# Kernel tuning notes

Measured on AMD Instinct MI355X. Metric: run time of the kernel, lower is better.

Reference implementation:

```python
import jax, jax.numpy as jnp
import numpy as np
from jax import lax

UNIT = 0.11  # pairing threshold from sort_w(weight, 0.11)


def _greedy_pairs(wflat, unit=UNIT):
    """Faithful greedy pairing from sort_w: for each out-channel dd, scan flat
    indices a ascending; pair a with the first unoccupied b>a with
    |w[a]+w[b]|<=unit. Returns gather indices src and signs such that
    Weff[dd,i] = sign[dd,i] * Wflat[dd, src[dd,i]] reproduces vicsum_v2."""
    d, m = wflat.shape
    src = np.tile(np.arange(m, dtype=np.int32), (d, 1))
    sign = np.ones((d, m), dtype=np.float32)
    for dd in range(d):
        occ = np.zeros(m, dtype=bool)
        row = wflat[dd]
        for a in range(m - 1):
            if occ[a]:
                continue
            cand = np.nonzero((~occ[a + 1:]) & (np.abs(row[a] + row[a + 1:]) <= unit))[0]
            if cand.size:
                b = a + 1 + int(cand[0])
                occ[a] = occ[b] = True
                src[dd, b] = a     # out += (x[a]-x[b])*w[a]  =>  coeff at b is -w[a]
                sign[dd, b] = -1.0
    return src, sign


def _make_conv(rng, d, c, k):
    bound = 1.0 / np.sqrt(c * k * k)  # torch default uniform init scale
    w = rng.uniform(-bound, bound, size=(d, c, k, k)).astype(np.float32)
    b = rng.uniform(-bound, bound, size=(d,)).astype(np.float32)
    src, sign = _greedy_pairs(w.reshape(d, -1))
    return w, b, src, sign


def setup_inputs() -> dict:
    rng = np.random.default_rng(0)
    x = rng.standard_normal((16384, 1, 32, 32)).astype(np.float32)
    w1, b1, src1, sign1 = _make_conv(rng, 6, 1, 5)
    w2, b2, src2, sign2 = _make_conv(rng, 16, 6, 5)
    w3, b3, src3, sign3 = _make_conv(rng, 120, 16, 5)
    bf1 = 1.0 / np.sqrt(120.0)
    fc1_w = rng.uniform(-bf1, bf1, size=(84, 120)).astype(np.float32)
    fc1_b = rng.uniform(-bf1, bf1, size=(84,)).astype(np.float32)
    bf2 = 1.0 / np.sqrt(84.0)
    fc2_w = rng.uniform(-bf2, bf2, size=(10, 84)).astype(np.float32)
    fc2_b = rng.uniform(-bf2, bf2, size=(10,)).astype(np.float32)
    return {
        'x': jnp.asarray(x),
        'w1': jnp.asarray(w1), 'b1': jnp.asarray(b1), 'sign1': jnp.asarray(sign1),
        'w2': jnp.asarray(w2), 'b2': jnp.asarray(b2), 'sign2': jnp.asarray(sign2),
        'w3': jnp.asarray(w3), 'b3': jnp.asarray(b3), 'sign3': jnp.asarray(sign3),
        'fc1_w': jnp.asarray(fc1_w), 'fc1_b': jnp.asarray(fc1_b),
        'fc2_w': jnp.asarray(fc2_w), 'fc2_b': jnp.asarray(fc2_b),
        'src1': jnp.asarray(src1), 'src2': jnp.asarray(src2), 'src3': jnp.asarray(src3),
        'TRIGGERed': 1, 'count': 0,
    }


def _eff_weight(w, src, sign):
    d = w.shape[0]
    wflat = w.reshape(d, -1)
    weff = jnp.take_along_axis(wflat, src, axis=1) * sign
    return weff.reshape(w.shape)


def _conv(x, w, b):
    y = lax.conv_general_dilated(x, w, window_strides=(1, 1), padding='VALID',
                                 dimension_numbers=('NCHW', 'OIHW', 'NCHW'))
    return y + b[None, :, None, None]


def _avgpool2(x):
    n, c, h, w = x.shape
    return x.reshape(n, c, h // 2, 2, w // 2, 2).mean(axis=(3, 5))


def reference(x, w1, b1, sign1, w2, b2, sign2, w3, b3, sign3,
              fc1_w, fc1_b, fc2_w, fc2_b, src1, src2, src3, TRIGGERed, count):
    if TRIGGERed:
        h = _avgpool2(jax.nn.sigmoid(_conv(x, _eff_weight(w1, src1, sign1), b1)))
        h = _avgpool2(jax.nn.sigmoid(_conv(h, _eff_weight(w2, src2, sign2), b2)))
        h = jax.nn.sigmoid(_conv(h, _eff_weight(w3, src3, sign3), b3))
    else:
        h = _avgpool2(jax.nn.sigmoid(_conv(x, w1, b1)))
        h = _avgpool2(jax.nn.sigmoid(_conv(h, w2, b2)))
        h = jax.nn.sigmoid(_conv(h, w3, b3))
    h = h.reshape(h.shape[0], -1)                     # [N, 120]
    h = jax.nn.sigmoid(h @ fc1_w.T + fc1_b)           # [N, 84]
    return h @ fc2_w.T + fc2_b                        # [N, 10]
```

## Files before the change

### kernel.cpp

```cpp
#include <hip/hip_runtime.h>

#define THREADS 256

typedef _Float16 half2v __attribute__((ext_vector_type(2)));
typedef __fp16   half2p __attribute__((ext_vector_type(2)));

__device__ __forceinline__ float sigmoidf(float x) {
    return __builtin_amdgcn_rcpf(1.0f + __expf(-x));
}

__device__ __forceinline__ half2v f2h2(float f) {
    union { float f; half2v h; } u; u.f = f; return u.h;
}

__device__ __forceinline__ half2v pk2h2(half2p p) {
    union { half2p p; half2v h; } u; u.p = p; return u.h;
}

#define E2OFF 168
#define E3OFF 2856
#define P1OFF 54056

__global__ void weff_prep(const float* __restrict__ w1, const float* __restrict__ sg1, const int* __restrict__ sr1,
                          const float* __restrict__ w2, const float* __restrict__ sg2, const int* __restrict__ sr2,
                          const float* __restrict__ w3, const float* __restrict__ sg3, const int* __restrict__ sr3,
                          const int* __restrict__ trig, float* __restrict__ ws) {
    int i = blockIdx.x * blockDim.x + threadIdx.x;
    const int t = trig[0];
    if (i < 168) {
        int c = i / 28, k = i % 28;
        float v = 0.f;
        if (k < 25) { int f = c * 25 + k; v = t ? sg1[f] * w1[c * 25 + sr1[f]] : w1[f]; }
        ws[i] = v;
    } else if (i < 1704) {
        int j = i - E2OFF;
        int oc = j / 96, r = j % 96, ic = r / 16, slot = r % 16;
        const int base = oc * 150 + ic * 25;
        float outv = 0.f;
        if (slot < 10) {
            int kx = slot >> 1, p = slot & 1;
            int k0 = base + (2 * p) * 5 + kx;
            int k1 = base + (2 * p + 1) * 5 + kx;
            float v0 = t ? sg2[k0] * w2[oc * 150 + sr2[k0]] : w2[k0];
            float v1 = t ? sg2[k1] * w2[oc * 150 + sr2[k1]] : w2[k1];
            union { _Float16 h[2]; float f; } pun;
            pun.h[0] = (_Float16)v0;
            pun.h[1] = (_Float16)v1;
            outv = pun.f;
        } else if (slot < 15) {
            int kx = slot - 10;
            int k4 = base + 20 + kx;
            outv = t ? sg2[k4] * w2[oc * 150 + sr2[k4]] : w2[k4];
        }
        ws[i] = outv;
    } else if (i < E3OFF) {
        ws[i] = 0.f;
    } else if (i < P1OFF) {
        int idx = i - E3OFF;
        if (idx < 48000) {
            int q  = idx & 3;
            int j  = (idx >> 2) & 1;
            int tt = (idx >> 3) % 120;
            int k  = idx / 960;
            int c  = 2 * (tt >> 1) + j;
            int h  = tt & 1;
            int e  = c * 400 + h * 200 + 4 * k + q;
            ws[i] = t ? sg3[e] * w3[c * 400 + sr3[e]] : w3[e];
        } else {
            ws[i] = 0.f;
        }
    }
}

__global__ __launch_bounds__(THREADS, 4)
void k_conv1(const float* __restrict__ x, const float* __restrict__ ws,
             const float* __restrict__ b1, float* __restrict__ p1, int nimg) {
    __shared__ __align__(16) float lw[176];
    const int tid = threadIdx.x;
    if (tid < 168) lw[tid] = ws[tid];
    if (tid >= 168 && tid < 174) lw[tid] = b1[tid - 168];
    __syncthreads();

    int g = blockIdx.x * THREADS + tid;
    if (g >= nimg * 98) return;
    const int img = g / 98, rem = g % 98;
    const int r = rem / 7, t = rem % 7;

    const float* xb = x + (size_t)img * 1024 + (2 * r) * 32 + 4 * t;
    float pt[6][8];
    #pragma unroll
    for (int rr = 0; rr < 6; ++rr) {
        const float4 v0 = *reinterpret_cast<const float4*>(xb + rr * 32);
        const float4 v1 = *reinterpret_cast<const float4*>(xb + rr * 32 + 4);
        pt[rr][0] = v0.x; pt[rr][1] = v0.y; pt[rr][2] = v0.z; pt[rr][3] = v0.w;
        pt[rr][4] = v1.x; pt[rr][5] = v1.y; pt[rr][6] = v1.z; pt[rr][7] = v1.w;
    }

    #pragma unroll
    for (int c = 0; c < 6; ++c) {
        float z[2][4];
        #pragma unroll
        for (int p = 0; p < 2; ++p)
            #pragma unroll
            for (int w = 0; w < 4; ++w) z[p][w] = 0.f;

        #pragma unroll
        for (int k4 = 0; k4 < 6; ++k4) {
            const float4 w4 = *reinterpret_cast<const float4*>(&lw[c * 28 + 4 * k4]);
            #pragma unroll
            for (int j = 0; j < 4; ++j) {
                const int k = 4 * k4 + j;
                const int ky = k / 5, kx = k % 5;
                const float wv = (j == 0) ? w4.x : (j == 1) ? w4.y : (j == 2) ? w4.z : w4.w;
                #pragma unroll
                for (int p = 0; p < 2; ++p)
                    #pragma unroll
                    for (int dy = 0; dy < 2; ++dy)
                        #pragma unroll
                        for (int dx = 0; dx < 2; ++dx)
                            z[p][2 * dy + dx] += pt[dy + ky][2 * p + dx + kx] * wv;
            }
        }
        {
            const float wv = lw[c * 28 + 24];
            #pragma unroll
            for (int p = 0; p < 2; ++p)
                #pragma unroll
                for (int dy = 0; dy < 2; ++dy)
                    #pragma unroll
                    for (int dx = 0; dx < 2; ++dx)
                        z[p][2 * dy + dx] += pt[dy + 4][2 * p + dx + 4] * wv;
        }

        const float bb = lw[168 + c];
        const float s0 = sigmoidf(z[0][0] + bb) + sigmoidf(z[0][1] + bb) +
                         sigmoidf(z[0][2] + bb) + sigmoidf(z[0][3] + bb);
        const float s1 = sigmoidf(z[1][0] + bb) + sigmoidf(z[1][1] + bb) +
                         sigmoidf(z[1][2] + bb) + sigmoidf(z[1][3] + bb);
        *reinterpret_cast<float2*>(&p1[((size_t)img * 6 + c) * 196 + r * 14 + 2 * t]) =
            make_float2(0.25f * s0, 0.25f * s1);
    }
}

__global__ __launch_bounds__(THREADS, 3)
void k_conv2(const float* __restrict__ p1, const float* __restrict__ ws,
             const float* __restrict__ b2, float* __restrict__ p2, int nimg) {
    int g = blockIdx.x * THREADS + threadIdx.x;
    if (g >= nimg * 50) return;
    const int img = g / 50, rem = g % 50;
    const int pix = rem >> 1, di = rem & 1;
    const int pi = pix / 5, pj = pix % 5;
    const float* pimg = p1 + (size_t)img * 1176 + (2 * pi + di) * 14 + 2 * pj;
    const float* wq = ws + E2OFF;

    float acc[16][2];
    #pragma unroll
    for (int oc = 0; oc < 16; ++oc) { acc[oc][0] = 0.f; acc[oc][1] = 0.f; }

    for (int ic = 0; ic < 6; ++ic) {
        float pt[5][6];
        const float* pb = pimg + ic * 196;
        #pragma unroll
        for (int r = 0; r < 5; ++r) {
            #pragma unroll
            for (int cc = 0; cc < 3; ++cc) {
                float2 v = *reinterpret_cast<const float2*>(pb + r * 14 + 2 * cc);
                pt[r][2 * cc] = v.x; pt[r][2 * cc + 1] = v.y;
            }
        }
        half2v pk01[6], pk23[6];
        #pragma unroll
        for (int cc = 0; cc < 6; ++cc) {
            pk01[cc] = pk2h2(__builtin_amdgcn_cvt_pkrtz(pt[0][cc], pt[1][cc]));
            pk23[cc] = pk2h2(__builtin_amdgcn_cvt_pkrtz(pt[2][cc], pt[3][cc]));
        }
        #pragma unroll
        for (int oc = 0; oc < 16; ++oc) {
            const float* wrow = wq + (oc * 6 + ic) * 16;
            #pragma unroll
            for (int kx = 0; kx < 5; ++kx) {
                const half2v wa = f2h2(wrow[2 * kx]);
                const half2v wb = f2h2(wrow[2 * kx + 1]);
                const float  wf = wrow[10 + kx];
                acc[oc][0] = __builtin_amdgcn_fdot2(pk01[kx], wa, acc[oc][0], false);
                acc[oc][0] = __builtin_amdgcn_fdot2(pk23[kx], wb, acc[oc][0], false);
                acc[oc][0] += pt[4][kx] * wf;
                acc[oc][1] = __builtin_amdgcn_fdot2(pk01[kx + 1], wa, acc[oc][1], false);
                acc[oc][1] = __builtin_amdgcn_fdot2(pk23[kx + 1], wb, acc[oc][1], false);
                acc[oc][1] += pt[4][kx + 1] * wf;
            }
        }
    }

    #pragma unroll
    for (int oc = 0; oc < 16; ++oc) {
        const float bb = b2[oc];
        float s = sigmoidf(acc[oc][0] + bb) + sigmoidf(acc[oc][1] + bb);
        s += __shfl_xor(s, 1, 64);
        if (di == 0)
            p2[(size_t)img * 400 + oc * 25 + pix] = 0.25f * s;
    }
}

#define T_IMG 8
__global__ __launch_bounds__(128, 4)
void k_tail(const float* __restrict__ p2, const float* __restrict__ ws,
            const float* __restrict__ b3,
            const float* __restrict__ fc1w, const float* __restrict__ fc1b,
            const float* __restrict__ fc2w, const float* __restrict__ fc2b,
            float* __restrict__ out, int nimg) {
    __shared__ __align__(16) float sp2[T_IMG][400];
    __shared__ __align__(16) float v3[T_IMG][120];
    __shared__ __align__(16) float v4[T_IMG][84];
    const int tid = threadIdx.x;
    const int img0 = blockIdx.x * T_IMG;

    for (int i = tid; i < T_IMG * 100; i += 128) {
        const int im = i / 100, off = i % 100;
        const int gi = min(img0 + im, nimg - 1);
        reinterpret_cast<float4*>(&sp2[im][0])[off] =
            reinterpret_cast<const float4*>(p2 + (size_t)gi * 400)[off];
    }
    __syncthreads();

    if (tid < 120) {
        const int h = tid & 1;
        const int cpair = tid >> 1;
        float acc[2][T_IMG];
        #pragma unroll
        for (int j = 0; j < 2; ++j)
            #pragma unroll
            for (int im = 0; im < T_IMG; ++im) acc[j][im] = 0.f;

        const float4* wp = reinterpret_cast<const float4*>(ws + E3OFF);
        #pragma unroll 2
        for (int k = 0; k < 50; ++k) {
            const float4 w0 = wp[(k * 120 + tid) * 2];
            const float4 w1 = wp[(k * 120 + tid) * 2 + 1];
            #pragma unroll
            for (int im = 0; im < T_IMG; ++im) {
                const float4 u = *reinterpret_cast<const float4*>(&sp2[im][h * 200 + 4 * k]);
                acc[0][im] += w0.x * u.x + w0.y * u.y + w0.z * u.z + w0.w * u.w;
                acc[1][im] += w1.x * u.x + w1.y * u.y + w1.z * u.z + w1.w * u.w;
            }
        }
        #pragma unroll
        for (int j = 0; j < 2; ++j) {
            const int c = 2 * cpair + j;
            const float bb = b3[c];
            #pragma unroll
            for (int im = 0; im < T_IMG; ++im) {
                float s = acc[j][im];
                s += __shfl_xor(s, 1, 64);
                if (h == 0) v3[im][c] = sigmoidf(s + bb);
            }
        }
    }
    __syncthreads();

    for (int it = tid; it < T_IMG * 84; it += 128) {
        const int im = it / 84, j = it % 84;
        const float4* wp = reinterpret_cast<const float4*>(fc1w + j * 120);
        const float4* vp = reinterpret_cast<const float4*>(&v3[im][0]);
        float4 a = make_float4(0.f, 0.f, 0.f, 0.f);
        #pragma unroll 6
        for (int k = 0; k < 30; ++k) {
            const float4 w4 = wp[k];
            const float4 u = vp[k];
            a.x += u.x * w4.x; a.y += u.y * w4.y;
            a.z += u.z * w4.z; a.w += u.w * w4.w;
        }
        v4[im][j] = sigmoidf((a.x + a.y) + (a.z + a.w) + fc1b[j]);
    }
    __syncthreads();

    if (tid < T_IMG * 10) {
        const int im = tid / 10, j = tid % 10;
        if (img0 + im < nimg) {
            const float4* wp = reinterpret_cast<const float4*>(fc2w + j * 84);
            const float4* vp = reinterpret_cast<const float4*>(&v4[im][0]);
            float4 a = make_float4(0.f, 0.f, 0.f, 0.f);
            #pragma unroll
            for (int k = 0; k < 21; ++k) {
                const float4 w4 = wp[k];
                const float4 u = vp[k];
                a.x += u.x * w4.x; a.y += u.y * w4.y;
                a.z += u.z * w4.z; a.w += u.w * w4.w;
            }
            out[(size_t)(img0 + im) * 10 + j] = (a.x + a.y) + (a.z + a.w) + fc2b[j];
        }
    }
}

__device__ __forceinline__ float wget_ig(const float* __restrict__ wp,
                                         const float* __restrict__ sg,
                                         const int* __restrict__ sr,
                                         int row, int m, int idx, bool tg) {
    int f = row * m + idx;
    return tg ? sg[f] * wp[row * m + sr[f]] : wp[f];
}

__global__ __launch_bounds__(THREADS, 4)
void lenet_fused(const float* __restrict__ x,
                 const float* __restrict__ w1e, const float* __restrict__ b1,
                 const float* __restrict__ w2e, const float* __restrict__ b2,
                 const float* __restrict__ w3e, const float* __restrict__ b3,
                 const float* __restrict__ fc1w, const float* __restrict__ fc1b,
                 const float* __restrict__ fc2w, const float* __restrict__ fc2b,
                 const float* __restrict__ sg1, const int* __restrict__ sr1,
                 const float* __restrict__ sg2, const int* __restrict__ sr2,
                 const float* __restrict__ sg3, const int* __restrict__ sr3,
                 const int* __restrict__ trig,
                 float* __restrict__ out, int nimg) {
    const int tid = threadIdx.x;
    const int img0 = blockIdx.x * 2;
    __shared__ __align__(16) float xs[2][1024];
    __shared__ __align__(16) float p1[2][6][196];
    __shared__ __align__(16) float p2[2][400];
    __shared__ __align__(16) float v3[2][120];
    __shared__ __align__(16) float v4[2][84];
    const bool tg = trig[0] != 0;

    #pragma unroll
    for (int im = 0; im < 2; ++im) {
        int gi = min(img0 + im, nimg - 1);
        reinterpret_cast<float4*>(&xs[im][0])[tid] =
            reinterpret_cast<const float4*>(x + (size_t)gi * 1024)[tid];
    }
    __syncthreads();

    for (int it = tid; it < 2 * 196; it += THREADS) {
        const int img = it / 196, pix = it % 196;
        const int pi = pix / 14, pj = pix % 14;
        const float* xb = &xs[img][(2 * pi) * 32 + 2 * pj];
        float pt[6][6];
        #pragma unroll
        for (int r = 0; r < 6; ++r)
            #pragma unroll
            for (int cc = 0; cc < 3; ++cc) {
                float2 v = *reinterpret_cast<const float2*>(&xb[r * 32 + cc * 2]);
                pt[r][cc * 2] = v.x; pt[r][cc * 2 + 1] = v.y;
            }
        #pragma unroll
        for (int c = 0; c < 6; ++c) {
            float z0 = 0.f, z1 = 0.f, z2 = 0.f, z3 = 0.f;
            #pragma unroll
            for (int ky = 0; ky < 5; ++ky)
                #pragma unroll
                for (int kx = 0; kx < 5; ++kx) {
                    const float wv = wget_ig(w1e, sg1, sr1, c, 25, ky * 5 + kx, tg);
                    z0 += pt[ky][kx] * wv;     z1 += pt[ky][kx + 1] * wv;
                    z2 += pt[ky + 1][kx] * wv; z3 += pt[ky + 1][kx + 1] * wv;
                }
            const float bb = b1[c];
            p1[img][c][pix] = 0.25f * (sigmoidf(z0 + bb) + sigmoidf(z1 + bb) +
                                       sigmoidf(z2 + bb) + sigmoidf(z3 + bb));
        }
    }
    __syncthreads();

    if (tid < 200) {
        const int img = tid / 100, rem = tid % 100;
        const int pix = rem >> 2, win = rem & 3;
        const int di = win >> 1, dj = win & 1;
        const int pi = pix / 5, pj = pix % 5;
        const int r0 = 2 * pi + di, c0 = 2 * pj + dj;
        float acc[16];
        #pragma unroll
        for (int c = 0; c < 16; ++c) acc[c] = 0.f;
        for (int ic = 0; ic < 6; ++ic) {
            float pt[5][5];
            #pragma unroll
            for (int ky = 0; ky < 5; ++ky)
                #pragma unroll
                for (int kx = 0; kx < 5; ++kx)
                    pt[ky][kx] = p1[img][ic][(r0 + ky) * 14 + (c0 + kx)];
            #pragma unroll
            for (int c = 0; c < 16; ++c) {
                float z = acc[c];
                #pragma unroll
                for (int ky = 0; ky < 5; ++ky)
                    #pragma unroll
                    for (int kx = 0; kx < 5; ++kx)
                        z += pt[ky][kx] * wget_ig(w2e, sg2, sr2, c, 150, ic * 25 + ky * 5 + kx, tg);
                acc[c] = z;
            }
        }
        #pragma unroll
        for (int c = 0; c < 16; ++c) {
            float z = sigmoidf(acc[c] + b2[c]);
            z += __shfl_xor(z, 1, 64);
            z += __shfl_xor(z, 2, 64);
            if (win == 0) p2[img][c * 25 + pix] = 0.25f * z;
        }
    }
    __syncthreads();

    if (tid < 240) {
        const int c = tid >> 1, h = tid & 1;
        float s0 = 0.f, s1 = 0.f;
        for (int k = 0; k < 200; ++k) {
            float wv = wget_ig(w3e, sg3, sr3, c, 400, h * 200 + k, tg);
            s0 += p2[0][h * 200 + k] * wv;
            s1 += p2[1][h * 200 + k] * wv;
        }
        s0 += __shfl_xor(s0, 1, 64);
        s1 += __shfl_xor(s1, 1, 64);
        if (h == 0) {
            const float bb = b3[c];
            v3[0][c] = sigmoidf(s0 + bb);
            v3[1][c] = sigmoidf(s1 + bb);
        }
    }
    __syncthreads();

    if (tid < 168) {
        const int img = tid / 84, j = tid % 84;
        float a = 0.f;
        for (int k = 0; k < 120; ++k) a += v3[img][k] * fc1w[j * 120 + k];
        v4[img][j] = sigmoidf(a + fc1b[j]);
    }
    __syncthreads();

    if (tid < 20) {
        const int img = tid / 10, j = tid % 10;
        if (img0 + img < nimg) {
            float a = 0.f;
            for (int k = 0; k < 84; ++k) a += v4[img][k] * fc2w[j * 84 + k];
            out[(size_t)(img0 + img) * 10 + j] = a + fc2b[j];
        }
    }
}

extern "C" void kernel_launch(void* const* d_in, const int* in_sizes, int n_in,
                              void* d_out, int out_size, void* d_ws, size_t ws_size,
                              hipStream_t stream) {
    const float* x    = (const float*)d_in[0];
    const float* w1   = (const float*)d_in[1];
    const float* b1   = (const float*)d_in[2];
    const float* sg1  = (const float*)d_in[3];
    const float* w2   = (const float*)d_in[4];
    const float* b2   = (const float*)d_in[5];
    const float* sg2  = (const float*)d_in[6];
    const float* w3   = (const float*)d_in[7];
    const float* b3   = (const float*)d_in[8];
    const float* sg3  = (const float*)d_in[9];
    const float* fc1w = (const float*)d_in[10];
    const float* fc1b = (const float*)d_in[11];
    const float* fc2w = (const float*)d_in[12];
    const float* fc2b = (const float*)d_in[13];
    const int*   sr1  = (const int*)d_in[14];
    const int*   sr2  = (const int*)d_in[15];
    const int*   sr3  = (const int*)d_in[16];
    const int*   trig = (const int*)d_in[17];

    const int nimg = in_sizes[0] / 1024;
    float* out = (float*)d_out;

    const size_t p1off = P1OFF;
    const size_t p2off = p1off + (size_t)nimg * 1176;
    const size_t need_bytes = (p2off + (size_t)nimg * 400) * sizeof(float);

    if (ws_size >= need_bytes) {
        float* ws = (float*)d_ws;
        weff_prep<<<(P1OFF + 255) / 256, 256, 0, stream>>>(
            w1, sg1, sr1, w2, sg2, sr2, w3, sg3, sr3, trig, ws);
        k_conv1<<<(nimg * 98 + THREADS - 1) / THREADS, THREADS, 0, stream>>>(
            x, ws, b1, ws + p1off, nimg);
        k_conv2<<<(nimg * 50 + THREADS - 1) / THREADS, THREADS, 0, stream>>>(
            ws + p1off, ws, b2, ws + p2off, nimg);
        k_tail<<<(nimg + T_IMG - 1) / T_IMG, 128, 0, stream>>>(
            ws + p2off, ws, b3, fc1w, fc1b, fc2w, fc2b, out, nimg);
    } else {
        lenet_fused<<<(nimg + 1) / 2, THREADS, 0, stream>>>(
            x, w1, b1, w2, b2, w3, b3,
            fc1w, fc1b, fc2w, fc2b, sg1, sr1, sg2, sr2, sg3, sr3, trig, out, nimg);
    }
}
```

Baseline: 220.0 us.

## Store conv2 pooled output as packed fp16 and use fdot2 in conv3

```diff
diff --git a/kernel.cpp b/kernel.cpp
--- a/kernel.cpp
+++ b/kernel.cpp
@@ -15,6 +15,10 @@
 
 __device__ __forceinline__ half2v pk2h2(half2p p) {
     union { half2p p; half2v h; } u; u.p = p; return u.h;
+}
+
+__device__ __forceinline__ float h2pf(half2p p) {
+    union { half2p p; float f; } u; u.p = p; return u.f;
 }
 
 #define E2OFF 168
@@ -55,20 +59,30 @@
         ws[i] = outv;
     } else if (i < E3OFF) {
         ws[i] = 0.f;
+    } else if (i < 26856) {
+        int idx = i - E3OFF;
+        int q   = idx & 3;
+        int ch  = (idx >> 2) & 1;
+        int tt  = (idx >> 3) % 120;
+        int j4  = idx / 960;
+        int h   = tt & 1;
+        int cpair = tt >> 1;
+        int c   = 2 * cpair + ch;
+        int s   = h * 100 + 4 * j4 + q;
+        int ocp = s / 25, pix = s % 25;
+        int e0  = (2 * ocp) * 25 + pix;
+        int e1  = (2 * ocp + 1) * 25 + pix;
+        float v0 = t ? sg3[c * 400 + e0 - (c * 400 + e0) + c * 400 + e0] * 0.f : 0.f;
+        int f0 = c * 400 + e0;
+        int f1 = c * 400 + e1;
+        v0 = t ? sg3[f0] * w3[c * 400 + sr3[f0]] : w3[f0];
+        float v1 = t ? sg3[f1] * w3[c * 400 + sr3[f1]] : w3[f1];
+        union { _Float16 hh[2]; float f; } pun;
+        pun.hh[0] = (_Float16)v0;
+        pun.hh[1] = (_Float16)v1;
+        ws[i] = pun.f;
     } else if (i < P1OFF) {
-        int idx = i - E3OFF;
-        if (idx < 48000) {
-            int q  = idx & 3;
-            int j  = (idx >> 2) & 1;
-            int tt = (idx >> 3) % 120;
-            int k  = idx / 960;
-            int c  = 2 * (tt >> 1) + j;
-            int h  = tt & 1;
-            int e  = c * 400 + h * 200 + 4 * k + q;
-            ws[i] = t ? sg3[e] * w3[c * 400 + sr3[e]] : w3[e];
-        } else {
-            ws[i] = 0.f;
-        }
+        ws[i] = 0.f;
     }
 }
 
@@ -144,7 +158,7 @@
 
 __global__ __launch_bounds__(THREADS, 3)
 void k_conv2(const float* __restrict__ p1, const float* __restrict__ ws,
-             const float* __restrict__ b2, float* __restrict__ p2, int nimg) {
+             const float* __restrict__ b2, float* __restrict__ p2h, int nimg) {
     int g = blockIdx.x * THREADS + threadIdx.x;
     if (g >= nimg * 50) return;
     const int img = g / 50, rem = g % 50;
@@ -192,34 +206,41 @@
         }
     }
 
+    float pooled[16];
     #pragma unroll
     for (int oc = 0; oc < 16; ++oc) {
         const float bb = b2[oc];
         float s = sigmoidf(acc[oc][0] + bb) + sigmoidf(acc[oc][1] + bb);
         s += __shfl_xor(s, 1, 64);
-        if (di == 0)
-            p2[(size_t)img * 400 + oc * 25 + pix] = 0.25f * s;
+        pooled[oc] = 0.25f * s;
+    }
+    if (di == 0) {
+        #pragma unroll
+        for (int ocp = 0; ocp < 8; ++ocp) {
+            p2h[(size_t)img * 200 + ocp * 25 + pix] =
+                h2pf(__builtin_amdgcn_cvt_pkrtz(pooled[2 * ocp], pooled[2 * ocp + 1]));
+        }
     }
 }
 
 #define T_IMG 8
 __global__ __launch_bounds__(128, 4)
-void k_tail(const float* __restrict__ p2, const float* __restrict__ ws,
+void k_tail(const float* __restrict__ p2h, const float* __restrict__ ws,
             const float* __restrict__ b3,
             const float* __restrict__ fc1w, const float* __restrict__ fc1b,
             const float* __restrict__ fc2w, const float* __restrict__ fc2b,
             float* __restrict__ out, int nimg) {
-    __shared__ __align__(16) float sp2[T_IMG][400];
+    __shared__ __align__(16) float sp2[T_IMG][200];
     __shared__ __align__(16) float v3[T_IMG][120];
     __shared__ __align__(16) float v4[T_IMG][84];
     const int tid = threadIdx.x;
     const int img0 = blockIdx.x * T_IMG;
 
-    for (int i = tid; i < T_IMG * 100; i += 128) {
-        const int im = i / 100, off = i % 100;
+    for (int i = tid; i < T_IMG * 50; i += 128) {
+        const int im = i / 50, off = i % 50;
         const int gi = min(img0 + im, nimg - 1);
         reinterpret_cast<float4*>(&sp2[im][0])[off] =
-            reinterpret_cast<const float4*>(p2 + (size_t)gi * 400)[off];
+            reinterpret_cast<const float4*>(p2h + (size_t)gi * 200)[off];
     }
     __syncthreads();
 
@@ -233,15 +254,20 @@
             for (int im = 0; im < T_IMG; ++im) acc[j][im] = 0.f;
 
         const float4* wp = reinterpret_cast<const float4*>(ws + E3OFF);
-        #pragma unroll 2
-        for (int k = 0; k < 50; ++k) {
-            const float4 w0 = wp[(k * 120 + tid) * 2];
-            const float4 w1 = wp[(k * 120 + tid) * 2 + 1];
+        for (int j4 = 0; j4 < 25; ++j4) {
+            const float4 w0 = wp[(j4 * 120 + tid) * 2];
+            const float4 w1 = wp[(j4 * 120 + tid) * 2 + 1];
             #pragma unroll
             for (int im = 0; im < T_IMG; ++im) {
-                const float4 u = *reinterpret_cast<const float4*>(&sp2[im][h * 200 + 4 * k]);
-                acc[0][im] += w0.x * u.x + w0.y * u.y + w0.z * u.z + w0.w * u.w;
-                acc[1][im] += w1.x * u.x + w1.y * u.y + w1.z * u.z + w1.w * u.w;
+                const float4 u = *reinterpret_cast<const float4*>(&sp2[im][h * 100 + 4 * j4]);
+                acc[0][im] = __builtin_amdgcn_fdot2(f2h2(u.x), f2h2(w0.x), acc[0][im], false);
+                acc[0][im] = __builtin_amdgcn_fdot2(f2h2(u.y), f2h2(w0.y), acc[0][im], false);
+                acc[0][im] = __builtin_amdgcn_fdot2(f2h2(u.z), f2h2(w0.z), acc[0][im], false);
+                acc[0][im] = __builtin_amdgcn_fdot2(f2h2(u.w), f2h2(w0.w), acc[0][im], false);
+                acc[1][im] = __builtin_amdgcn_fdot2(f2h2(u.x), f2h2(w1.x), acc[1][im], false);
+                acc[1][im] = __builtin_amdgcn_fdot2(f2h2(u.y), f2h2(w1.y), acc[1][im], false);
+                acc[1][im] = __builtin_amdgcn_fdot2(f2h2(u.z), f2h2(w1.z), acc[1][im], false);
+                acc[1][im] = __builtin_amdgcn_fdot2(f2h2(u.w), f2h2(w1.w), acc[1][im], false);
             }
         }
         #pragma unroll
@@ -459,7 +485,7 @@
 
     const size_t p1off = P1OFF;
     const size_t p2off = p1off + (size_t)nimg * 1176;
-    const size_t need_bytes = (p2off + (size_t)nimg * 400) * sizeof(float);
+    const size_t need_bytes = (p2off + (size_t)nimg * 200) * sizeof(float);
 
     if (ws_size >= need_bytes) {
         float* ws = (float*)d_ws;
```

After: 231.7 us. 5.3% more time.
